# Performance work log

Measured on AMD Instinct MI355X. Metric: run time of the kernel, lower is better.

## Reference

```python
import jax, jax.numpy as jnp
import numpy as np

N, M, BS = 32, 64, 512
ALPHA, BETA = 1.0, 1.0


def setup_inputs() -> dict:
    key = jax.random.key(0)
    k1, k2, k3, k4 = jax.random.split(key, 4)
    q = jax.random.normal(k1, (BS, N), jnp.float32)
    b = jax.random.normal(k2, (BS, M), jnp.float32)
    A0 = jax.random.normal(k3, (N, N), jnp.float32)
    P = A0 @ A0.T / N + jnp.eye(N, dtype=jnp.float32)  # SPD cost matrix
    H = jax.random.normal(k4, (M, N), jnp.float32) / jnp.sqrt(jnp.float32(N))
    return {"q": q, "b": b, "P": P, "H": H, "iters": 1000}


def reference(q, b, P, H, iters):
    m = H.shape[0]
    # Pinv-applied quantities via solve (matches torch.linalg.solve / pinv usage)
    Pinv_q = jnp.linalg.solve(P, q.T).T                 # (bs, n)
    D = H @ jnp.linalg.solve(P, H.T)                    # (m, m) = H P^-1 H^T
    # dummy preconditioner: scaled identity keeping the operator nonexpansive
    lam_max = jnp.linalg.eigvalsh(D)[-1]
    tD = (BETA / lam_max) * jnp.eye(m, dtype=q.dtype)   # (m, m)
    mu = ((H @ Pinv_q.T).T - b) @ tD.T                  # (bs, m)
    tDD = tD @ D
    I = jnp.eye(m, dtype=q.dtype)
    A = jnp.block([[tDD, tD],
                   [-2.0 * ALPHA * tDD + I, I - 2.0 * ALPHA * tD]])  # (2m, 2m)
    B = jnp.concatenate([mu, -2.0 * ALPHA * mu], axis=1)             # (bs, 2m)
    Hinv = jnp.linalg.pinv(H)                            # (n, m)
    X0 = jnp.zeros((q.shape[0], 2 * m), q.dtype)

    def step(X, _):
        X = X @ A.T + B
        X = X.at[:, m:].set(jax.nn.relu(X[:, m:]))       # in-place ReLU on dual half
        return X, X

    _, ys = jax.lax.scan(step, X0, None, length=iters)   # (iters, bs, 2m)
    Xs = jnp.concatenate([X0[None], ys], axis=0).transpose(1, 0, 2)  # (bs, iters+1, 2m)
    # primal_sols[k] = Hinv @ (X_k[m:] - b)
    primal_sols = jnp.einsum('nm,bkm->bkn', Hinv, Xs[:, :, m:] - b[:, None, :])
    return Xs, primal_sols
```

## Files before the change

### kernel.cpp

```cpp
#include <hip/hip_runtime.h>
#include <math.h>

#define BATCH 512
#define ITERS 1000
#define PLEN 25
#define PHASES 40

typedef float f32x2 __attribute__((ext_vector_type(2)));
typedef float f32x4 __attribute__((ext_vector_type(4)));

__device__ __forceinline__ float rdlane(float v, int l) {
  return __int_as_float(__builtin_amdgcn_readlane(__float_as_int(v), l));
}
__device__ __forceinline__ f32x2 fma2(f32x2 a, f32x2 b, f32x2 c) {
#if __has_builtin(__builtin_elementwise_fma)
  return __builtin_elementwise_fma(a, b, c);
#else
  f32x2 r; r.x = fmaf(a.x, b.x, c.x); r.y = fmaf(a.y, b.y, c.y); return r;
#endif
}

#define DC(c) (((c) & 1) ? dcol2[(c) >> 1].y : dcol2[(c) >> 1].x)

#define GJ32_REG(g)                                            \
  _Pragma("unroll")                                            \
  for (int k = 0; k < 32; ++k) {                               \
    float inv = 1.0f / rdlane(g[k], k);                        \
    g[k] *= inv;                                               \
    _Pragma("unroll")                                          \
    for (int ii = 0; ii < 32; ++ii) {                          \
      if (ii == k) continue;                                   \
      float f = rdlane(g[ii], k);                              \
      g[ii] = fmaf(-f, g[k], g[ii]);                           \
    }                                                          \
  }

__global__ __launch_bounds__(128, 1)
void fused_kernel(const float* __restrict__ q,
                  const float* __restrict__ bmat,
                  const float* __restrict__ P,
                  const float* __restrict__ H,
                  float* __restrict__ Xs,
                  float* __restrict__ out2) {
  __shared__ __align__(16) float stage[2112];
  __shared__ __align__(16) float X1R[2][PLEN][64];
  __shared__ __align__(16) float X2R[2][PLEN][64];

  const int tid = threadIdx.x;
  const int wv = tid >> 6;
  const int lane = tid & 63;
  const int row = blockIdx.x;
  const int i = lane & 31, h = lane >> 5;

  float hreg[32];
  {
    const f32x4* hp = (const f32x4*)(H + lane * 32);
    #pragma unroll
    for (int j4 = 0; j4 < 8; ++j4) {
      f32x4 t = hp[j4];
      hreg[4*j4+0] = t.x; hreg[4*j4+1] = t.y; hreg[4*j4+2] = t.z; hreg[4*j4+3] = t.w;
    }
  }
  const float bl = bmat[row * 64 + lane];

  f32x2 dcol2[32]; float s = 0.f, mu = 0.f;
  f32x4 xb[16];
  float x1 = 0.f, x2 = 0.f;
  f32x2 hv2[16];
  float* Xp = Xs + (size_t)row * (ITERS + 1) * 128;
  float* ob = out2 + (size_t)row * (ITERS + 1) * 32;

  if (wv == 1) {
    #pragma unroll
    for (int j = 0; j < 32; ++j) stage[lane * 33 + j] = hreg[j];
  }
  __syncthreads();
  float gB[32];
  if (wv == 1) {
    float htc[64];
    #pragma unroll
    for (int m = 0; m < 64; ++m) htc[m] = stage[m * 33 + i];
    #pragma unroll
    for (int r = 0; r < 32; ++r) {
      float a0 = 0.f, a1 = 0.f;
      #pragma unroll
      for (int m = 0; m < 64; m += 2) {
        a0 = fmaf(rdlane(hreg[r], m),     htc[m],     a0);
        a1 = fmaf(rdlane(hreg[r], m + 1), htc[m + 1], a1);
      }
      float hth = a0 + a1;
      gB[r] = (lane < 32) ? hth : (((lane - 32) == r) ? 1.0f : 0.0f);
    }
    GJ32_REG(gB)
  }
  __syncthreads();
  if (wv == 1) {
    #pragma unroll
    for (int r = 0; r < 32; ++r) {
      float a0 = 0.f, a1 = 0.f;
      #pragma unroll
      for (int c = 0; c < 32; c += 2) {
        a0 = fmaf(rdlane(gB[r], 32 + c),     hreg[c],     a0);
        a1 = fmaf(rdlane(gB[r], 32 + c + 1), hreg[c + 1], a1);
      }
      stage[r * 66 + lane] = a0 + a1;
    }
  }
  __syncthreads();
  if (wv == 1) {
    #pragma unroll
    for (int t = 0; t < 16; ++t)
      hv2[t] = *(const f32x2*)&stage[i * 66 + 32 * h + 2 * t];
  }

  if (wv == 0) {
    float pht[32], acc;
    {
      float g[32];
      #pragma unroll
      for (int r = 0; r < 32; ++r) {
        float pv = P[r * 32 + i];
        g[r] = (lane < 32) ? pv : (((lane - 32) == r) ? 1.0f : 0.0f);
      }
      GJ32_REG(g)
      #pragma unroll
      for (int r = 0; r < 32; ++r) {
        float a0 = 0.f, a1 = 0.f;
        #pragma unroll
        for (int j = 0; j < 32; j += 2) {
          a0 = fmaf(rdlane(g[r], 32 + j),     hreg[j],     a0);
          a1 = fmaf(rdlane(g[r], 32 + j + 1), hreg[j + 1], a1);
        }
        pht[r] = a0 + a1;
      }
    }
    {
      const float* qp = q + row * 32;
      float a0 = 0.f, a1 = 0.f;
      #pragma unroll
      for (int r = 0; r < 32; r += 2) {
        a0 = fmaf(qp[r],     pht[r],     a0);
        a1 = fmaf(qp[r + 1], pht[r + 1], a1);
      }
      acc = a0 + a1;
    }
    #pragma unroll
    for (int r = 0; r < 64; ++r) {
      float a0 = 0.f, a1 = 0.f;
      #pragma unroll
      for (int j = 0; j < 32; j += 2) {
        a0 = fmaf(rdlane(hreg[j],     r), pht[j],     a0);
        a1 = fmaf(rdlane(hreg[j + 1], r), pht[j + 1], a1);
      }
      float val = a0 + a1;
      if (r & 1) dcol2[r >> 1].y = val; else dcol2[r >> 1].x = val;
    }
    {
      float ecol[64];
      #pragma unroll
      for (int r = 0; r < 64; ++r) {
        float a0 = 0.f, a1 = 0.f;
        #pragma unroll
        for (int c = 0; c < 64; c += 2) {
          a0 = fmaf(rdlane(DC(r), c),     DC(c),     a0);
          a1 = fmaf(rdlane(DC(r), c + 1), DC(c + 1), a1);
        }
        ecol[r] = a0 + a1;
      }
      float v = 1.0f + 0.017f * (float)lane;
      #pragma unroll 1
      for (int t = 0; t < 112; ++t) {
        float a0 = 0.f, a1 = 0.f, a2 = 0.f, a3 = 0.f;
        #pragma unroll
        for (int c = 0; c < 64; c += 4) {
          a0 = fmaf(ecol[c+0], rdlane(v, c+0), a0);
          a1 = fmaf(ecol[c+1], rdlane(v, c+1), a1);
          a2 = fmaf(ecol[c+2], rdlane(v, c+2), a2);
          a3 = fmaf(ecol[c+3], rdlane(v, c+3), a3);
        }
        v = (a0 + a1) + (a2 + a3);
        if ((t & 7) == 7) {
          float n2 = v * v;
          #pragma unroll
          for (int m = 1; m < 64; m <<= 1) n2 += __shfl_xor(n2, m);
          v *= 1.0f / sqrtf(n2);
        }
      }
      float a0 = 0.f, a1 = 0.f, a2 = 0.f, a3 = 0.f;
      #pragma unroll
      for (int c = 0; c < 64; c += 4) {
        a0 = fmaf(DC(c+0), rdlane(v, c+0), a0);
        a1 = fmaf(DC(c+1), rdlane(v, c+1), a1);
        a2 = fmaf(DC(c+2), rdlane(v, c+2), a2);
        a3 = fmaf(DC(c+3), rdlane(v, c+3), a3);
      }
      float w = (a0 + a1) + (a2 + a3);
      float num = w * v, den = v * v;
      #pragma unroll
      for (int m = 1; m < 64; m <<= 1) {
        num += __shfl_xor(num, m);
        den += __shfl_xor(den, m);
      }
      s = den / num;
    }
    mu = s * (acc - bl);
    #pragma unroll
    for (int t = 0; t < 32; ++t) dcol2[t] *= s;

    x1 = mu;
    x2 = fmaxf(-2.0f * mu, 0.f);
    X1R[0][0][lane] = x1;
    X2R[0][0][lane] = x2 - bl;
    {
      const f32x4* bp = (const f32x4*)&X1R[0][0][0];
      #pragma unroll
      for (int t = 0; t < 16; ++t) xb[t] = bp[t];
    }
  }

  #pragma unroll 1
  for (int p = 0; p < PHASES; ++p) {
    if (wv == 0) {
      float* rx1 = &X1R[p & 1][0][0];
      float* rx2 = &X2R[p & 1][0][0];
      #pragma unroll 1
      for (int u = (p == 0) ? 1 : 0; u < PLEN; ++u) {
        float ta = fmaf(s, x2, mu);
        f32x2 A0 = {0.f, 0.f}, A1 = {0.f, 0.f};
        f32x2 A2 = {0.f, 0.f}, A3 = {0.f, 0.f};
        #pragma unroll
        for (int t = 0; t < 16; t += 2) {
          A0 = fma2(dcol2[2*t + 0], xb[t].xy,     A0);
          A1 = fma2(dcol2[2*t + 1], xb[t].zw,     A1);
          A2 = fma2(dcol2[2*t + 2], xb[t + 1].xy, A2);
          A3 = fma2(dcol2[2*t + 3], xb[t + 1].zw, A3);
        }
        f32x2 R = (A0 + A1) + (A2 + A3);
        float x1n = (R.x + R.y) + ta;
        rx1[u * 64 + lane] = x1n;
        {
          const f32x4* bp = (const f32x4*)(rx1 + u * 64);
          #pragma unroll
          for (int t = 0; t < 16; ++t) xb[t] = bp[t];
        }
        float x2n = fmaxf(fmaf(-2.0f, x1n, x1 + x2), 0.f);
        rx2[u * 64 + lane] = x2n - bl;
        x1 = x1n; x2 = x2n;
      }
    } else {
      if (p == 0) {
        Xp[lane] = 0.f;
        Xp[64 + lane] = 0.f;
        f32x2 pa = {0.f, 0.f}, pb = {0.f, 0.f};
        #pragma unroll
        for (int t = 0; t < 8; ++t) {
          f32x2 ta, tb;
          ta.x = -__shfl(bl, 32*h + 4*t + 0, 64);
          ta.y = -__shfl(bl, 32*h + 4*t + 1, 64);
          tb.x = -__shfl(bl, 32*h + 4*t + 2, 64);
          tb.y = -__shfl(bl, 32*h + 4*t + 3, 64);
          pa = fma2(hv2[2*t],     ta, pa);
          pb = fma2(hv2[2*t + 1], tb, pb);
        }
        float pr = (pa.x + pa.y) + (pb.x + pb.y);
        pr += __shfl_xor(pr, 32);
        if (h == 0) ob[i] = pr;
      } else {
        const float* rx1 = &X1R[(p - 1) & 1][0][0];
        const float* rx2 = &X2R[(p - 1) & 1][0][0];
        const int k0 = PLEN * (p - 1) + 1;
        float* Xk = Xp + (size_t)k0 * 128;
        float* obk = ob + (size_t)k0 * 32;
        #pragma unroll 1
        for (int u = 0; u < PLEN; ++u) {
          float x1v = rx1[u * 64 + lane];
          float x2mb = rx2[u * 64 + lane];
          Xk[u * 128 + lane] = x1v;
          Xk[u * 128 + 64 + lane] = x2mb + bl;
          const f32x4* tp = (const f32x4*)(rx2 + u * 64 + h * 32);
          f32x2 pa = {0.f, 0.f}, pb = {0.f, 0.f};
          #pragma unroll
          for (int t = 0; t < 8; ++t) {
            f32x4 tv = tp[t];
            pa = fma2(hv2[2*t],     tv.xy, pa);
            pb = fma2(hv2[2*t + 1], tv.zw, pb);
          }
          float pr = (pa.x + pa.y) + (pb.x + pb.y);
          pr += __shfl_xor(pr, 32);
          if (h == 0) obk[u * 32 + i] = pr;
        }
      }
    }
    __syncthreads();
  }

  if (wv == 1) {
    const float* rx1 = &X1R[1][0][0];
    const float* rx2 = &X2R[1][0][0];
    const int k0 = PLEN * (PHASES - 1) + 1;
    float* Xk = Xp + (size_t)k0 * 128;
    float* obk = ob + (size_t)k0 * 32;
    #pragma unroll 1
    for (int u = 0; u < PLEN; ++u) {
      float x1v = rx1[u * 64 + lane];
      float x2mb = rx2[u * 64 + lane];
      Xk[u * 128 + lane] = x1v;
      Xk[u * 128 + 64 + lane] = x2mb + bl;
      const f32x4* tp = (const f32x4*)(rx2 + u * 64 + h * 32);
      f32x2 pa = {0.f, 0.f}, pb = {0.f, 0.f};
      #pragma unroll
      for (int t = 0; t < 8; ++t) {
        f32x4 tv = tp[t];
        pa = fma2(hv2[2*t],     tv.xy, pa);
        pb = fma2(hv2[2*t + 1], tv.zw, pb);
      }
      float pr = (pa.x + pa.y) + (pb.x + pb.y);
      pr += __shfl_xor(pr, 32);
      if (h == 0) obk[u * 32 + i] = pr;
    }
  }
}

extern "C" void kernel_launch(void* const* d_in, const int* in_sizes, int n_in,
                              void* d_out, int out_size, void* d_ws, size_t ws_size,
                              hipStream_t stream) {
  (void)in_sizes; (void)n_in; (void)out_size; (void)d_ws; (void)ws_size;
  const float* q = (const float*)d_in[0];
  const float* b = (const float*)d_in[1];
  const float* P = (const float*)d_in[2];
  const float* H = (const float*)d_in[3];
  float* Xs = (float*)d_out;
  float* out2 = Xs + (size_t)BATCH * (ITERS + 1) * 128;

  fused_kernel<<<BATCH, 128, 0, stream>>>(q, b, P, H, Xs, out2);
}
```

Measured before the change: 577.4 us.

## Advance two recurrence steps per LDS round trip using precomputed D^2 operator

The serial recurrence loop now computes two iterations per pass. It precomputes s^2·D^2 columns and a constant offset c2, so the second step's matvec comes from the same shared-memory broadcast of the previous state as the first. This halves the LDS write-then-read synchronization points on the serial critical path, at the cost of roughly 1.5x the FMAs per step and extra registers for the second operator column. The phase length also changes from 25 to 20 steps with 50 phases, so each phase holds an even number of steps.

Result: slower. 886.0 us (+53.5%).

```diff
diff --git a/kernel.cpp b/kernel.cpp
--- a/kernel.cpp
+++ b/kernel.cpp
@@ -3,8 +3,8 @@
 
 #define BATCH 512
 #define ITERS 1000
-#define PLEN 25
-#define PHASES 40
+#define PLEN 20
+#define PHASES 50
 
 typedef float f32x2 __attribute__((ext_vector_type(2)));
 typedef float f32x4 __attribute__((ext_vector_type(4)));
@@ -63,8 +63,9 @@
   }
   const float bl = bmat[row * 64 + lane];
 
-  f32x2 dcol2[32]; float s = 0.f, mu = 0.f;
-  f32x4 xb[16];
+  f32x2 dcol2[32];
+  f32x2 d2col2[32];
+  float s = 0.f, mu = 0.f, c2 = 0.f;
   float x1 = 0.f, x2 = 0.f;
   f32x2 hv2[16];
   float* Xp = Xs + (size_t)row * (ITERS + 1) * 128;
@@ -115,6 +116,7 @@
 
   if (wv == 0) {
     float pht[32], acc;
+    float ecol[64];
     {
       float g[32];
       #pragma unroll
@@ -156,7 +158,6 @@
       if (r & 1) dcol2[r >> 1].y = val; else dcol2[r >> 1].x = val;
     }
     {
-      float ecol[64];
       #pragma unroll
       for (int r = 0; r < 64; ++r) {
         float a0 = 0.f, a1 = 0.f;
@@ -206,16 +207,27 @@
     mu = s * (acc - bl);
     #pragma unroll
     for (int t = 0; t < 32; ++t) dcol2[t] *= s;
-
-    x1 = mu;
-    x2 = fmaxf(-2.0f * mu, 0.f);
-    X1R[0][0][lane] = x1;
-    X2R[0][0][lane] = x2 - bl;
-    {
-      const f32x4* bp = (const f32x4*)&X1R[0][0][0];
-      #pragma unroll
-      for (int t = 0; t < 16; ++t) xb[t] = bp[t];
-    }
+    {
+      const float s2 = s * s;
+      #pragma unroll
+      for (int r = 0; r < 64; ++r) {
+        float v = s2 * ecol[r];
+        if (r & 1) d2col2[r >> 1].y = v; else d2col2[r >> 1].x = v;
+      }
+    }
+    {
+      float sdb = 0.f, sdmu = 0.f;
+      #pragma unroll
+      for (int c = 0; c < 64; c += 2) {
+        sdb  = fmaf(DC(c),     rdlane(bl, c),     sdb);
+        sdmu = fmaf(DC(c),     rdlane(mu, c),     sdmu);
+        sdb  = fmaf(DC(c + 1), rdlane(bl, c + 1), sdb);
+        sdmu = fmaf(DC(c + 1), rdlane(mu, c + 1), sdmu);
+      }
+      c2 = fmaf(s, sdb, sdmu) + mu;
+    }
+    X1R[1][PLEN - 1][lane] = 0.f;
+    X2R[1][PLEN - 1][lane] = -bl;
   }
 
   #pragma unroll 1
@@ -223,29 +235,38 @@
     if (wv == 0) {
       float* rx1 = &X1R[p & 1][0][0];
       float* rx2 = &X2R[p & 1][0][0];
+      const f32x4* pb1 = (const f32x4*)&X1R[(p ^ 1) & 1][PLEN - 1][0];
+      const f32x4* pb2 = (const f32x4*)&X2R[(p ^ 1) & 1][PLEN - 1][0];
       #pragma unroll 1
-      for (int u = (p == 0) ? 1 : 0; u < PLEN; ++u) {
-        float ta = fmaf(s, x2, mu);
-        f32x2 A0 = {0.f, 0.f}, A1 = {0.f, 0.f};
-        f32x2 A2 = {0.f, 0.f}, A3 = {0.f, 0.f};
-        #pragma unroll
-        for (int t = 0; t < 16; t += 2) {
-          A0 = fma2(dcol2[2*t + 0], xb[t].xy,     A0);
-          A1 = fma2(dcol2[2*t + 1], xb[t].zw,     A1);
-          A2 = fma2(dcol2[2*t + 2], xb[t + 1].xy, A2);
-          A3 = fma2(dcol2[2*t + 3], xb[t + 1].zw, A3);
-        }
-        f32x2 R = (A0 + A1) + (A2 + A3);
-        float x1n = (R.x + R.y) + ta;
-        rx1[u * 64 + lane] = x1n;
-        {
-          const f32x4* bp = (const f32x4*)(rx1 + u * 64);
-          #pragma unroll
-          for (int t = 0; t < 16; ++t) xb[t] = bp[t];
-        }
-        float x2n = fmaxf(fmaf(-2.0f, x1n, x1 + x2), 0.f);
-        rx2[u * 64 + lane] = x2n - bl;
-        x1 = x1n; x2 = x2n;
+      for (int j = 0; j < PLEN / 2; ++j) {
+        f32x2 M1a = {0.f,0.f}, M1b = {0.f,0.f};
+        f32x2 M2a = {0.f,0.f}, M2b = {0.f,0.f};
+        f32x2 M3a = {0.f,0.f}, M3b = {0.f,0.f};
+        #pragma unroll
+        for (int t = 0; t < 16; ++t) {
+          f32x4 v1 = pb1[t];
+          M1a = fma2(dcol2[2*t],    v1.xy, M1a);
+          M1b = fma2(dcol2[2*t+1],  v1.zw, M1b);
+          M2a = fma2(d2col2[2*t],   v1.xy, M2a);
+          M2b = fma2(d2col2[2*t+1], v1.zw, M2b);
+          f32x4 v2 = pb2[t];
+          M3a = fma2(dcol2[2*t],    v2.xy, M3a);
+          M3b = fma2(dcol2[2*t+1],  v2.zw, M3b);
+        }
+        f32x2 R1 = M1a + M1b; float m1 = R1.x + R1.y;
+        f32x2 R2 = M2a + M2b; float m2 = R2.x + R2.y;
+        f32x2 R3 = M3a + M3b; float m3 = R3.x + R3.y;
+        float x1k1 = m1 + fmaf(s, x2, mu);
+        float x2k1 = fmaxf(fmaf(-2.0f, x1k1, x1 + x2), 0.f);
+        float x1k2 = fmaf(s, m3 + x2k1, m2 + c2);
+        float x2k2 = fmaxf(fmaf(-2.0f, x1k2, x1k1 + x2k1), 0.f);
+        rx1[(2*j)     * 64 + lane] = x1k1;
+        rx2[(2*j)     * 64 + lane] = x2k1 - bl;
+        rx1[(2*j + 1) * 64 + lane] = x1k2;
+        rx2[(2*j + 1) * 64 + lane] = x2k2 - bl;
+        pb1 = (const f32x4*)(rx1 + (2*j + 1) * 64);
+        pb2 = (const f32x4*)(rx2 + (2*j + 1) * 64);
+        x1 = x1k2; x2 = x2k2;
       }
     } else {
       if (p == 0) {
```

## Split recurrence matvec across wave halves with permlane32 swap exchange

Applied to the files above, without the earlier changes.

Each lane now reads only the 32 x1 values belonging to its half-wave from LDS instead of all 64. It computes its own partial dot plus the partial for the partner lane in the other half, then exchanges that partial with v_permlane32_swap. The aim is to halve the LDS read traffic on the serial critical path of each iteration. The cost is an extra cross-lane swap per step and more registers (dA/dB), and the xchg32 trick of (a+b)-v may introduce rounding differences.

Measured after the change: 914.7 us. 58.4% more time.

```diff
diff --git a/kernel.cpp b/kernel.cpp
--- a/kernel.cpp
+++ b/kernel.cpp
@@ -18,6 +18,12 @@
 #else
   f32x2 r; r.x = fmaf(a.x, b.x, c.x); r.y = fmaf(a.y, b.y, c.y); return r;
 #endif
+}
+__device__ __forceinline__ float xchg32(float v) {
+  float a, b;
+  asm("v_mov_b32 %0, %2\n\tv_mov_b32 %1, %2" : "=&v"(a), "=&v"(b) : "v"(v));
+  asm volatile("v_permlane32_swap_b32 %0, %1" : "+v"(a), "+v"(b));
+  return (a + b) - v;
 }
 
 #define DC(c) (((c) & 1) ? dcol2[(c) >> 1].y : dcol2[(c) >> 1].x)
@@ -63,8 +69,10 @@
   }
   const float bl = bmat[row * 64 + lane];
 
-  f32x2 dcol2[32]; float s = 0.f, mu = 0.f;
-  f32x4 xb[16];
+  f32x2 dcol2[32];
+  f32x2 dA[16], dB[16];
+  float s = 0.f, mu = 0.f;
+  f32x4 xb[8];
   float x1 = 0.f, x2 = 0.f;
   f32x2 hv2[16];
   float* Xp = Xs + (size_t)row * (ITERS + 1) * 128;
@@ -207,14 +215,24 @@
     #pragma unroll
     for (int t = 0; t < 32; ++t) dcol2[t] *= s;
 
+    #pragma unroll
+    for (int t = 0; t < 16; ++t) {
+      dA[t] = h ? dcol2[16 + t] : dcol2[t];
+      f32x2 cx = h ? dcol2[t] : dcol2[16 + t];
+      f32x2 r;
+      r.x = xchg32(cx.x);
+      r.y = xchg32(cx.y);
+      dB[t] = r;
+    }
+
     x1 = mu;
     x2 = fmaxf(-2.0f * mu, 0.f);
     X1R[0][0][lane] = x1;
     X2R[0][0][lane] = x2 - bl;
     {
-      const f32x4* bp = (const f32x4*)&X1R[0][0][0];
-      #pragma unroll
-      for (int t = 0; t < 16; ++t) xb[t] = bp[t];
+      const f32x4* bp = (const f32x4*)(&X1R[0][0][0] + h * 32);
+      #pragma unroll
+      for (int t = 0; t < 8; ++t) xb[t] = bp[t];
     }
   }
 
@@ -226,22 +244,30 @@
       #pragma unroll 1
       for (int u = (p == 0) ? 1 : 0; u < PLEN; ++u) {
         float ta = fmaf(s, x2, mu);
-        f32x2 A0 = {0.f, 0.f}, A1 = {0.f, 0.f};
-        f32x2 A2 = {0.f, 0.f}, A3 = {0.f, 0.f};
-        #pragma unroll
-        for (int t = 0; t < 16; t += 2) {
-          A0 = fma2(dcol2[2*t + 0], xb[t].xy,     A0);
-          A1 = fma2(dcol2[2*t + 1], xb[t].zw,     A1);
-          A2 = fma2(dcol2[2*t + 2], xb[t + 1].xy, A2);
-          A3 = fma2(dcol2[2*t + 3], xb[t + 1].zw, A3);
-        }
-        f32x2 R = (A0 + A1) + (A2 + A3);
-        float x1n = (R.x + R.y) + ta;
+        f32x2 A0 = {0.f,0.f}, A1 = {0.f,0.f}, A2 = {0.f,0.f}, A3 = {0.f,0.f};
+        f32x2 B0 = {0.f,0.f}, B1 = {0.f,0.f}, B2 = {0.f,0.f}, B3 = {0.f,0.f};
+        #pragma unroll
+        for (int t = 0; t < 8; t += 2) {
+          A0 = fma2(dA[2*t + 0], xb[t].xy,     A0);
+          A1 = fma2(dA[2*t + 1], xb[t].zw,     A1);
+          A2 = fma2(dA[2*t + 2], xb[t + 1].xy, A2);
+          A3 = fma2(dA[2*t + 3], xb[t + 1].zw, A3);
+          B0 = fma2(dB[2*t + 0], xb[t].xy,     B0);
+          B1 = fma2(dB[2*t + 1], xb[t].zw,     B1);
+          B2 = fma2(dB[2*t + 2], xb[t + 1].xy, B2);
+          B3 = fma2(dB[2*t + 3], xb[t + 1].zw, B3);
+        }
+        f32x2 RA = (A0 + A1) + (A2 + A3);
+        f32x2 RB = (B0 + B1) + (B2 + B3);
+        float pown = RA.x + RA.y;
+        float poth = RB.x + RB.y;
+        float prec = xchg32(poth);
+        float x1n = (pown + prec) + ta;
         rx1[u * 64 + lane] = x1n;
         {
-          const f32x4* bp = (const f32x4*)(rx1 + u * 64);
+          const f32x4* bp = (const f32x4*)(rx1 + u * 64 + h * 32);
           #pragma unroll
-          for (int t = 0; t < 16; ++t) xb[t] = bp[t];
+          for (int t = 0; t < 8; ++t) xb[t] = bp[t];
         }
         float x2n = fmaxf(fmaf(-2.0f, x1n, x1 + x2), 0.f);
         rx2[u * 64 + lane] = x2n - bl;
```
